# Performance work log

Measured on AMD Instinct MI355X. Metric: run time of the kernel, lower is better.

Reference implementation:

```python
import jax, jax.numpy as jnp
import numpy as np

N, L, C_IN, NOISE_C, COMP, NC = 64, 1024, 514, 64, 16, 3
MAIN_C = COMP + NOISE_C  # 80

def _conv1d(x, w, b):
    # x: [N, Cin, L], w: [Cout, Cin, K] -> 'same' padding conv, stride 1
    k = w.shape[-1]
    y = jax.lax.conv_general_dilated(x, w, (1,), [(k // 2, k // 2)],
                                     dimension_numbers=('NCH', 'OIH', 'NCH'))
    return y + b[None, :, None]

def _bn(x, gamma, beta, eps=1e-5):
    # training-mode BatchNorm1d: biased batch stats over (N, L)
    mu = jnp.mean(x, axis=(0, 2), keepdims=True)
    var = jnp.var(x, axis=(0, 2), keepdims=True)
    return (x - mu) * jax.lax.rsqrt(var + eps) * gamma[None, :, None] + beta[None, :, None]

def _lrelu(x):
    return jax.nn.leaky_relu(x, 0.2)

def _pos_encode(length, dim, dtype):
    d = jnp.arange(dim)
    div = 1.0 / jnp.power(10000.0, (2.0 * (d // 2).astype(dtype)) / dim)  # [dim]
    ang = div[:, None] * jnp.arange(length, dtype=dtype)[None, :]          # [dim, L]
    pe = jnp.where((d % 2 == 0)[:, None], jnp.sin(ang), jnp.cos(ang))
    return pe[None].astype(dtype)  # [1, dim, L]

def _label_revise(probs):
    # Vectorized equivalent of the per-sample Python revision loop
    # (circle_itv=2, slider_itv=4, stride=2). Output length == input length.
    # Row j semantics (m = 4*(j//4), chain(m) = pred[m]==2 and pred[m+4]==2 and m+4<L):
    #   j%4==0: always probs[j]
    #   chain(m) and j%4!=0: pad [0,0,1]
    #   j%4==1 (not chain): pred[m] in {1,2} -> [1,0,0] else probs[j]
    #   j%4==2 (not chain): probs[j]
    #   j%4==3 (not chain): pred[j-1]==1 -> [1,0,0] else probs[j]
    n, l, c = probs.shape
    pred = jnp.argmax(probs, axis=-1)                 # [N, L]
    pred_b = pred[:, ::4]                              # pred at multiples of 4
    nxt = jnp.concatenate([pred_b[:, 1:], jnp.full((n, 1), -1, pred_b.dtype)], axis=1)
    chain = jnp.repeat((pred_b == 2) & (nxt == 2), 4, axis=1)   # [N, L]
    predm = jnp.repeat(pred_b, 4, axis=1)                        # [N, L]
    phase = jnp.arange(l) % 4
    prev = jnp.concatenate([jnp.zeros((n, 1), pred.dtype), pred[:, :-1]], axis=1)
    pad100 = jnp.array([1.0, 0.0, 0.0], probs.dtype)
    pad001 = jnp.array([0.0, 0.0, 1.0], probs.dtype)
    c100 = (((phase == 1)[None] & ((predm == 1) | (predm == 2)))
            | ((phase == 3)[None] & (prev == 1))) & ~chain
    out = jnp.where(c100[..., None], pad100, probs)
    out = jnp.where((chain & (phase != 0)[None])[..., None], pad001, out)
    return out

def _forward(noise, cond_data, gumbel, ew1, eb1, ew2, eb2, eg, ebt,
             w3, b3, w4, b4, g4, bt4, lw1, lb1, lw2, lb2, lw3, lb3):
    # FeatureExtractor
    x = jnp.swapaxes(cond_data, 1, 2)                       # [N, 514, L]
    x = _lrelu(_conv1d(x, ew1, eb1))                        # [N, 32, L]
    cond = _bn(_conv1d(x, ew2, eb2), eg, ebt)               # [N, 16, L] (no act)
    # main generator
    gi = jnp.concatenate([cond, jnp.swapaxes(noise, 1, 2)], axis=1)  # [N, 80, L]
    gi = gi + _pos_encode(L, MAIN_C, gi.dtype)
    h = _lrelu(_conv1d(gi, w3, b3))                         # [N, 48, L]
    h = _lrelu(_bn(_conv1d(h, w4, b4), g4, bt4))            # [N, 12, L]
    h = h.reshape(h.shape[0], -1)                           # [N, 12*L]
    h = _lrelu(h @ lw1 + lb1)
    h = _lrelu(h @ lw2 + lb2)
    logits = (h @ lw3 + lb3).reshape(-1, L, NC)             # [N, L, 3]
    rev = _label_revise(logits)
    # hard gumbel-softmax (tau=1) with straight-through estimator
    y_soft = jax.nn.softmax(rev + gumbel, axis=-1)
    y_hard = jax.nn.one_hot(jnp.argmax(y_soft, axis=-1), NC, dtype=y_soft.dtype)
    gen = y_hard + y_soft - jax.lax.stop_gradient(y_soft)
    return gen, cond

def setup_inputs() -> dict:
    key = jax.random.key(0)
    ks = jax.random.split(key, 12)
    s = jnp.float32(0.02)
    return {
        'noise': jax.random.normal(ks[0], (N, L, NOISE_C), jnp.float32),
        'cond_data': jax.random.normal(ks[1], (N, L, C_IN), jnp.float32),
        'gumbel': jax.random.gumbel(ks[2], (N, L, NC), jnp.float32),
        'ew1': jax.random.normal(ks[3], (C_IN // 16, C_IN, 1), jnp.float32) * s,
        'eb1': jnp.zeros((C_IN // 16,), jnp.float32),
        'ew2': jax.random.normal(ks[4], (COMP, C_IN // 16, 3), jnp.float32) * s,
        'eb2': jnp.zeros((COMP,), jnp.float32),
        'eg': jnp.ones((COMP,), jnp.float32),
        'ebt': jnp.zeros((COMP,), jnp.float32),
        'w3': jax.random.normal(ks[5], (NC * 16, MAIN_C, 7), jnp.float32) * s,
        'b3': jnp.zeros((NC * 16,), jnp.float32),
        'w4': jax.random.normal(ks[6], (NC * 4, NC * 16, 3), jnp.float32) * s,
        'b4': jnp.zeros((NC * 4,), jnp.float32),
        'g4': jnp.ones((NC * 4,), jnp.float32),
        'bt4': jnp.zeros((NC * 4,), jnp.float32),
        'lw1': jax.random.normal(ks[7], (NC * 4 * L, NC * L), jnp.float32) * s,
        'lb1': jnp.zeros((NC * L,), jnp.float32),
        'lw2': jax.random.normal(ks[8], (NC * L, NC * L), jnp.float32) * s,
        'lb2': jnp.zeros((NC * L,), jnp.float32),
        'lw3': jax.random.normal(ks[9], (NC * L, NC * L), jnp.float32) * s,
        'lb3': jnp.zeros((NC * L,), jnp.float32),
    }

def reference(noise, cond_data, gumbel, ew1, eb1, ew2, eb2, eg, ebt,
              w3, b3, w4, b4, g4, bt4, lw1, lb1, lw2, lb2, lw3, lb3):
    return _forward(noise, cond_data, gumbel, ew1, eb1, ew2, eb2, eg, ebt,
                    w3, b3, w4, b4, g4, bt4, lw1, lb1, lw2, lb2, lw3, lb3)
```

## Files before the change

### kernel.cpp

```cpp
#include <hip/hip_runtime.h>
#include <hip/hip_bf16.h>
#include <math.h>


__device__ __forceinline__ float lrelu(float x){ return fmaxf(x, 0.2f*x); }

__global__ void k_init(const float* __restrict__ ew1, const float* __restrict__ ew2,
                       const float* __restrict__ w3,  const float* __restrict__ w4,
                       float* __restrict__ wT1, float* __restrict__ wT2,
                       float* __restrict__ wT3, float* __restrict__ wT4,
                       float* __restrict__ pe){
  int i = blockIdx.x*256 + threadIdx.x;
  if (i < 16448){
    int c = i>>5, oc = i&31;
    wT1[i] = ew1[oc*514 + c];
  } else if (i < 16448+1536){
    int j = i - 16448; int oc = j%16; int t = j/16; int dl = t%3; int ic = t/3;
    wT2[j] = ew2[(oc*32+ic)*3 + dl];
  } else if (i < 16448+1536+26880){
    int j = i - 17984; int oc = j%48; int t = j/48; int dl = t%7; int ic = t/7;
    wT3[j] = w3[(oc*80+ic)*7 + dl];
  } else if (i < 46592){
    int j = i - 44864; int oc = j%12; int t = j/12; int dl = t%3; int ic = t/3;
    wT4[j] = w4[(oc*48+ic)*3 + dl];
  } else if (i < 46592 + 80*1024){
    int j = i - 46592;
    int ch = j >> 10, l = j & 1023;
    double dv = 1.0 / pow(10000.0, (2.0*(double)(ch>>1)) / 80.0);
    double ang = dv * (double)l;
    pe[j] = (float)((ch & 1) ? cos(ang) : sin(ang));
  }
}

__global__ __launch_bounds__(256) void k_conv1(const float* __restrict__ A,
    const float* __restrict__ wT1, const float* __restrict__ eb1,
    float* __restrict__ x1){
  __shared__ float red[32][256];
  const int tid = threadIdx.x;
  const int pl  = tid & 63;
  const int s   = __builtin_amdgcn_readfirstlane(tid >> 6);
  const int p   = blockIdx.x*64 + pl;

  const int c0 = (s == 0) ? 0 : 130 + (s-1)*128;
  const int c1 = (s == 0) ? 130 : 130 + s*128;

  const float* row = A + (size_t)p*514;
  float acc[32];
  #pragma unroll
  for (int j=0;j<32;j++) acc[j]=0.f;

  #pragma unroll 8
  for (int c=c0;c<c1;c+=2){
    float2 v = *reinterpret_cast<const float2*>(row + c);
    const float* w = wT1 + (size_t)c*32;
    #pragma unroll
    for (int j=0;j<32;j++) acc[j] = fmaf(v.x, w[j],    acc[j]);
    #pragma unroll
    for (int j=0;j<32;j++) acc[j] = fmaf(v.y, w[32+j], acc[j]);
  }

  #pragma unroll
  for (int j=0;j<32;j++) red[j][s*64 + pl] = acc[j];
  __syncthreads();

  float out[8];
  #pragma unroll
  for (int j=0;j<8;j++){
    const int c = s*8 + j;
    float v = (red[c][pl] + red[c][64+pl]) + (red[c][128+pl] + red[c][192+pl]);
    out[j] = lrelu(v + eb1[c]);
  }
  float* dst = x1 + ((size_t)(blockIdx.x*64 + pl))*32 + s*8;
  *(float4*)(dst  ) = make_float4(out[0],out[1],out[2],out[3]);
  *(float4*)(dst+4) = make_float4(out[4],out[5],out[6],out[7]);
}

__global__ __launch_bounds__(256) void k_conv2(const float* __restrict__ x1,
    const float* __restrict__ wT2, const float* __restrict__ eb2,
    float* __restrict__ y2, float* __restrict__ part){
  __shared__ float xt[32][264];
  const int tid = threadIdx.x, lane = tid & 63;
  const int wv = __builtin_amdgcn_readfirstlane(tid >> 6);
  const int n = blockIdx.x >> 2, base = (blockIdx.x & 3)*256;

  for (int r = tid; r < 264; r += 256){
    int l = base - 4 + r;
    if (l >= 0 && l < 1024){
      const float* src = x1 + ((size_t)n*1024 + l)*32;
      #pragma unroll
      for (int c=0;c<32;c+=4){
        float4 v = *(const float4*)(src + c);
        xt[c][r]=v.x; xt[c+1][r]=v.y; xt[c+2][r]=v.z; xt[c+3][r]=v.w;
      }
    } else {
      #pragma unroll
      for (int c=0;c<32;c++) xt[c][r] = 0.f;
    }
  }
  __syncthreads();

  const int og = wv*4;
  const int j0 = 4*lane;
  float acc[4][4];
  #pragma unroll
  for (int j=0;j<4;j++){
    #pragma unroll
    for (int p=0;p<4;p++) acc[j][p]=0.f;
  }
  for (int ic=0; ic<32; ic++){
    float xr[12];
    #pragma unroll
    for (int u=0;u<12;u+=4){
      float4 v = *(const float4*)&xt[ic][j0+u];
      xr[u]=v.x; xr[u+1]=v.y; xr[u+2]=v.z; xr[u+3]=v.w;
    }
    const float* wrow = wT2 + ic*48 + og;
    #pragma unroll
    for (int dl=0;dl<3;dl++){
      #pragma unroll
      for (int j=0;j<4;j++){
        float w = wrow[dl*16 + j];
        #pragma unroll
        for (int p=0;p<4;p++)
          acc[j][p] = fmaf(xr[p+dl+3], w, acc[j][p]);
      }
    }
  }
  float s[4], q[4];
  #pragma unroll
  for (int j=0;j<4;j++){ s[j]=0.f; q[j]=0.f; }
  const int l0 = base + 4*lane;
  #pragma unroll
  for (int p=0;p<4;p++){
    float vv[4];
    #pragma unroll
    for (int j=0;j<4;j++){
      float val = acc[j][p] + eb2[og+j];
      vv[j]=val; s[j]+=val; q[j]+=val*val;
    }
    *(float4*)(y2 + ((size_t)n*1024 + l0 + p)*16 + og) = make_float4(vv[0],vv[1],vv[2],vv[3]);
  }
  #pragma unroll
  for (int off=32; off; off>>=1){
    #pragma unroll
    for (int j=0;j<4;j++){ s[j] += __shfl_xor(s[j], off); q[j] += __shfl_xor(q[j], off); }
  }
  if (lane == 0){
    #pragma unroll
    for (int j=0;j<4;j++){
      part[((size_t)blockIdx.x*16 + og + j)*2    ] = s[j];
      part[((size_t)blockIdx.x*16 + og + j)*2 + 1] = q[j];
    }
  }
}

__global__ __launch_bounds__(256) void k_gi(const float* __restrict__ y2,
    const float* __restrict__ noise, const float* __restrict__ pe,
    const float* __restrict__ bn2p, const float* __restrict__ eg,
    const float* __restrict__ ebt,
    float* __restrict__ gi, float* __restrict__ cond_out){
  __shared__ double pS[16][16], pQ[16][16];
  __shared__ float ssh[32];
  const int tid = threadIdx.x;
  {
    int c = tid & 15, chunk = tid >> 4;
    double S=0.0, Q=0.0;
    #pragma unroll 4
    for (int i=chunk*16; i<chunk*16+16; i++){
      S += (double)bn2p[((size_t)i*16 + c)*2];
      Q += (double)bn2p[((size_t)i*16 + c)*2 + 1];
    }
    pS[chunk][c] = S; pQ[chunk][c] = Q;
  }
  __syncthreads();
  if (tid < 16){
    double S=0.0, Q=0.0;
    #pragma unroll
    for (int k=0;k<16;k++){ S += pS[k][tid]; Q += pQ[k][tid]; }
    double mean = S / 65536.0;
    double var  = Q / 65536.0 - mean*mean;
    double sc   = (double)eg[tid] / sqrt(var + 1e-5);
    ssh[tid*2]   = (float)sc;
    ssh[tid*2+1] = (float)((double)ebt[tid] - mean*sc);
  }
  __syncthreads();

  int n = blockIdx.x >> 2;
  int l = (blockIdx.x & 3)*256 + tid;
  size_t p = (size_t)n*1024 + l;
  float* grow = gi + p*80;
  #pragma unroll
  for (int c=0;c<16;c++){
    float v  = y2[p*16 + c];
    float cv = fmaf(v, ssh[2*c], ssh[2*c+1]);
    cond_out[((size_t)n*16 + c)*1024 + l] = cv;
    grow[c] = cv + pe[c*1024 + l];
  }
  #pragma unroll
  for (int c=0;c<64;c++){
    grow[16+c] = noise[p*64 + c] + pe[(16+c)*1024 + l];
  }
}

__global__ __launch_bounds__(256) void k_conv3(const float* __restrict__ gi,
    const float* __restrict__ wT3, const float* __restrict__ b3,
    float* __restrict__ h3){
  __shared__ float xt[80][136];
  const int tid = threadIdx.x, lane = tid & 63;
  const int og = __builtin_amdgcn_readfirstlane(tid >> 6) * 12;
  const int n = blockIdx.x >> 3, base = (blockIdx.x & 7)*128;

  {
    const int half = tid & 1;
    for (int r = tid >> 1; r < 136; r += 128){
      int l = base - 4 + r;
      if (l >= 0 && l < 1024){
        const float* src = gi + ((size_t)n*1024 + l)*80 + half*40;
        #pragma unroll
        for (int c=0;c<40;c+=4){
          float4 v = *(const float4*)(src + c);
          xt[half*40+c][r]=v.x; xt[half*40+c+1][r]=v.y; xt[half*40+c+2][r]=v.z; xt[half*40+c+3][r]=v.w;
        }
      } else {
        #pragma unroll
        for (int c=0;c<40;c++) xt[half*40+c][r]=0.f;
      }
    }
  }
  __syncthreads();

  float acc[12][2];
  #pragma unroll
  for (int j=0;j<12;j++){ acc[j][0]=0.f; acc[j][1]=0.f; }
  const int j0 = 2*lane;
  for (int ic=0; ic<80; ic++){
    float xr[10];
    #pragma unroll
    for (int u=0;u<10;u+=2){
      float2 v = *(const float2*)&xt[ic][j0+u];
      xr[u]=v.x; xr[u+1]=v.y;
    }
    const float* wrow = wT3 + ic*336 + og;
    #pragma unroll
    for (int dl=0;dl<7;dl++){
      #pragma unroll
      for (int j=0;j<12;j++){
        float w = wrow[dl*48 + j];
        acc[j][0] = fmaf(xr[1+dl], w, acc[j][0]);
        acc[j][1] = fmaf(xr[2+dl], w, acc[j][1]);
      }
    }
  }
  const int l0 = base + 2*lane;
  #pragma unroll
  for (int p=0;p<2;p++){
    float v[12];
    #pragma unroll
    for (int j=0;j<12;j++) v[j] = lrelu(acc[j][p] + b3[og+j]);
    float* dst = h3 + ((size_t)n*1024 + l0 + p)*48 + og;
    *(float4*)(dst  ) = make_float4(v[0],v[1],v[2],v[3]);
    *(float4*)(dst+4) = make_float4(v[4],v[5],v[6],v[7]);
    *(float4*)(dst+8) = make_float4(v[8],v[9],v[10],v[11]);
  }
}

__global__ __launch_bounds__(256) void k_conv4(const float* __restrict__ h3,
    const float* __restrict__ wT4, const float* __restrict__ b4,
    float* __restrict__ y4, float* __restrict__ part){
  __shared__ float xt[48][258];
  __shared__ float red[4][24];
  const int tid = threadIdx.x, lane = tid & 63, wv = tid >> 6;
  const int n = blockIdx.x >> 2, base = (blockIdx.x & 3)*256;

  for (int r = tid; r < 258; r += 256){
    int l = base - 1 + r;
    if (l >= 0 && l < 1024){
      const float* src = h3 + ((size_t)n*1024 + l)*48;
      #pragma unroll
      for (int c=0;c<48;c+=4){
        float4 v = *(const float4*)(src + c);
        xt[c][r]=v.x; xt[c+1][r]=v.y; xt[c+2][r]=v.z; xt[c+3][r]=v.w;
      }
    } else {
      #pragma unroll
      for (int c=0;c<48;c++) xt[c][r]=0.f;
    }
  }
  __syncthreads();

  float acc[12];
  #pragma unroll
  for (int j=0;j<12;j++) acc[j]=0.f;
  for (int ic=0; ic<48; ic++){
    float x0 = xt[ic][tid], x1v = xt[ic][tid+1], x2 = xt[ic][tid+2];
    const float* wrow = wT4 + ic*36;
    #pragma unroll
    for (int j=0;j<12;j++){
      acc[j] = fmaf(x0,  wrow[j],      acc[j]);
      acc[j] = fmaf(x1v, wrow[12 + j], acc[j]);
      acc[j] = fmaf(x2,  wrow[24 + j], acc[j]);
    }
  }
  float s[12], q[12];
  #pragma unroll
  for (int j=0;j<12;j++){
    float v = acc[j] + b4[j];
    acc[j] = v; s[j] = v; q[j] = v*v;
  }
  {
    float* dst = y4 + ((size_t)n*1024 + base + tid)*12;
    *(float4*)(dst  ) = make_float4(acc[0],acc[1],acc[2],acc[3]);
    *(float4*)(dst+4) = make_float4(acc[4],acc[5],acc[6],acc[7]);
    *(float4*)(dst+8) = make_float4(acc[8],acc[9],acc[10],acc[11]);
  }
  #pragma unroll
  for (int off=32; off; off>>=1){
    #pragma unroll
    for (int j=0;j<12;j++){ s[j] += __shfl_xor(s[j], off); q[j] += __shfl_xor(q[j], off); }
  }
  if (lane == 0){
    #pragma unroll
    for (int j=0;j<12;j++){ red[wv][j] = s[j]; red[wv][12+j] = q[j]; }
  }
  __syncthreads();
  if (tid < 24){
    float v = red[0][tid] + red[1][tid] + red[2][tid] + red[3][tid];
    if (tid < 12) part[((size_t)blockIdx.x*12 + tid)*2] = v;
    else          part[((size_t)blockIdx.x*12 + (tid-12))*2 + 1] = v;
  }
}

__global__ __launch_bounds__(256) void k_hflat(const float* __restrict__ y4,
    const float* __restrict__ bn4p, const float* __restrict__ g4,
    const float* __restrict__ bt4, float* __restrict__ hT){
  __shared__ double pS[16][12], pQ[16][12];
  __shared__ float ssh[24];
  const int tid = threadIdx.x;
  if (tid < 192){
    int c = tid % 12, chunk = tid / 12;
    double S=0.0, Q=0.0;
    #pragma unroll 4
    for (int i=chunk*16; i<chunk*16+16; i++){
      S += (double)bn4p[((size_t)i*12 + c)*2];
      Q += (double)bn4p[((size_t)i*12 + c)*2 + 1];
    }
    pS[chunk][c] = S; pQ[chunk][c] = Q;
  }
  __syncthreads();
  if (tid < 12){
    double S=0.0, Q=0.0;
    #pragma unroll
    for (int k=0;k<16;k++){ S += pS[k][tid]; Q += pQ[k][tid]; }
    double mean = S / 65536.0;
    double var  = Q / 65536.0 - mean*mean;
    double sc   = (double)g4[tid] / sqrt(var + 1e-5);
    ssh[tid*2]   = (float)sc;
    ssh[tid*2+1] = (float)((double)bt4[tid] - mean*sc);
  }
  __syncthreads();

  int nn = tid & 63;
  int l  = blockIdx.x*4 + (tid >> 6);
  const float* src = y4 + ((size_t)nn*1024 + l)*12;
  #pragma unroll
  for (int c=0;c<12;c++){
    float v = lrelu(fmaf(src[c], ssh[2*c], ssh[2*c+1]));
    hT[((size_t)(c*1024 + l))*64 + nn] = v;
  }
}

__global__ __launch_bounds__(256) void k_fc2(const float* __restrict__ AT,
    const float* __restrict__ W, float* __restrict__ part,
    int nsplit, int kwave){
  __shared__ float red[64][64];
  const int lane = threadIdx.x & 63;
  const int w  = __builtin_amdgcn_readfirstlane(threadIdx.x >> 6);
  const int sk = w >> 1;
  const int mh = (w & 1) * 32;
  const int s  = blockIdx.x % nsplit;
  const int ot = blockIdx.x / nsplit;
  const int o  = ot*64 + lane;
  const int k0 = (s*2 + sk) * kwave;

  float acc[32];
  #pragma unroll
  for (int m=0;m<32;m++) acc[m]=0.f;

  const float* ap = AT + (size_t)k0*64 + mh;
  const float* wp = W  + (size_t)k0*3072 + o;

  float wb[8];
  #pragma unroll
  for (int u=0;u<8;u++) wb[u] = wp[(size_t)u*3072];

  for (int k=0; k<kwave-8; k+=8){
    float wn[8];
    const float* wpn = wp + (size_t)(k+8)*3072;
    #pragma unroll
    for (int u=0;u<8;u++) wn[u] = wpn[(size_t)u*3072];
    #pragma unroll
    for (int u=0;u<8;u++){
      const float* a = ap + (size_t)(k+u)*64;
      #pragma unroll
      for (int m=0;m<32;m++) acc[m] = fmaf(a[m], wb[u], acc[m]);
    }
    #pragma unroll
    for (int u=0;u<8;u++) wb[u] = wn[u];
  }
  #pragma unroll
  for (int u=0;u<8;u++){
    const float* a = ap + (size_t)(kwave-8+u)*64;
    #pragma unroll
    for (int m=0;m<32;m++) acc[m] = fmaf(a[m], wb[u], acc[m]);
  }

  if (sk == 1){
    #pragma unroll
    for (int m=0;m<32;m++) red[mh + m][lane] = acc[m];
  }
  __syncthreads();
  if (sk == 0){
    float* dst = part + (size_t)s*64*3072 + o;
    #pragma unroll
    for (int m=0;m<32;m++){
      acc[m] += red[mh + m][lane];
      dst[(size_t)(mh + m)*3072] = acc[m];
    }
  }
}

__global__ __launch_bounds__(256) void k_fcreduce(const float* __restrict__ part,
    const float* __restrict__ bias, float* __restrict__ out,
    int S, int act, int transposed){
  const int ot = blockIdx.x >> 4;
  const int mg = blockIdx.x & 15;
  const int lane = threadIdx.x & 63;
  const int o = ot*64 + lane;
  const int m = mg*4 + (threadIdx.x >> 6);
  float v = 0.f;
  for (int s=0;s<S;s++) v += part[((size_t)s*64 + m)*3072 + o];
  v += bias[o];
  if (act) v = fmaxf(v, 0.2f*v);
  if (transposed) out[(size_t)o*64 + m] = v;
  else            out[(size_t)m*3072 + o] = v;
}

__global__ __launch_bounds__(256) void k_label(const float* __restrict__ logits,
    const float* __restrict__ gumbel, float* __restrict__ out){
  __shared__ int pred[1024];
  const int n = blockIdx.x;
  const float* lg = logits + (size_t)n*3072;
  for (int l = threadIdx.x; l < 1024; l += 256){
    float a = lg[l*3], b = lg[l*3+1], c = lg[l*3+2];
    int pm = 0; float bv = a;
    if (b > bv){ pm = 1; bv = b; }
    if (c > bv){ pm = 2; }
    pred[l] = pm;
  }
  __syncthreads();
  const float* gm = gumbel + (size_t)n*3072;
  float* op = out + (size_t)n*3072;
  for (int l = threadIdx.x; l < 1024; l += 256){
    int phase = l & 3, lb = l >> 2;
    int pb  = pred[lb*4];
    int nxt = (lb < 255) ? pred[(lb+1)*4] : -1;
    bool chain = (pb == 2) && (nxt == 2);
    int prev = (l > 0) ? pred[l-1] : 0;
    bool c100 = (((phase == 1) && (pb == 1 || pb == 2)) ||
                 ((phase == 3) && (prev == 1))) && !chain;
    float r0, r1, r2;
    if (chain && phase != 0){ r0=0.f; r1=0.f; r2=1.f; }
    else if (c100)          { r0=1.f; r1=0.f; r2=0.f; }
    else { r0 = lg[l*3]; r1 = lg[l*3+1]; r2 = lg[l*3+2]; }
    float z0 = r0 + gm[l*3], z1 = r1 + gm[l*3+1], z2 = r2 + gm[l*3+2];
    int am = 0; float bv = z0;
    if (z1 > bv){ am = 1; bv = z1; }
    if (z2 > bv){ am = 2; }
    op[l*3+0] = (am == 0) ? 1.f : 0.f;
    op[l*3+1] = (am == 1) ? 1.f : 0.f;
    op[l*3+2] = (am == 2) ? 1.f : 0.f;
  }
}

extern "C" void kernel_launch(void* const* d_in, const int* in_sizes, int n_in,
                              void* d_out, int out_size, void* d_ws, size_t ws_size,
                              hipStream_t stream){
  (void)in_sizes; (void)n_in; (void)out_size;
  const float* noise     = (const float*)d_in[0];
  const float* cond_data = (const float*)d_in[1];
  const float* gumbel    = (const float*)d_in[2];
  const float* ew1 = (const float*)d_in[3];
  const float* eb1 = (const float*)d_in[4];
  const float* ew2 = (const float*)d_in[5];
  const float* eb2 = (const float*)d_in[6];
  const float* eg  = (const float*)d_in[7];
  const float* ebt = (const float*)d_in[8];
  const float* w3  = (const float*)d_in[9];
  const float* b3  = (const float*)d_in[10];
  const float* w4  = (const float*)d_in[11];
  const float* b4  = (const float*)d_in[12];
  const float* g4  = (const float*)d_in[13];
  const float* bt4 = (const float*)d_in[14];
  const float* lw1 = (const float*)d_in[15];
  const float* lb1 = (const float*)d_in[16];
  const float* lw2 = (const float*)d_in[17];
  const float* lb2 = (const float*)d_in[18];
  const float* lw3 = (const float*)d_in[19];
  const float* lb3 = (const float*)d_in[20];

  float* ws = (float*)d_ws;
  float* wT1   = ws + 0;
  float* wT2   = ws + 16448;
  float* wT3   = ws + 17984;
  float* wT4   = ws + 44864;
  float* pe    = ws + 46592;
  float* bn2p  = ws + 128512;
  float* bn4p  = ws + 136736;
  float* x1    = ws + 143360;
  float* y2    = ws + 2240512;
  float* h3    = ws + 143360;
  float* gi    = ws + 3289088;
  float* y4    = ws + 3289088;
  float* hT    = ws + 4075520;
  float* fcp   = ws + 4861952;

  int S1 = 32;
  if (ws_size < (size_t)(4861952 + 32*196608 + 3*196608) * 4) S1 = 16;
  const int S23 = 16;
  float* fc1T  = fcp + (size_t)S1*196608;
  float* fc2T  = fc1T + 196608;
  float* logi  = fc2T + 196608;
  const int kw1  = 12288 / (S1*2);
  const int kw23 = 3072 / (S23*2);

  float* out_gen  = (float*)d_out;
  float* out_cond = (float*)d_out + 196608;

  k_init <<<502, 256, 0, stream>>>(ew1, ew2, w3, w4, wT1, wT2, wT3, wT4, pe);
  k_conv1<<<1024, 256, 0, stream>>>(cond_data, wT1, eb1, x1);
  k_conv2<<<256, 256, 0, stream>>>(x1, wT2, eb2, y2, bn2p);
  k_gi   <<<256, 256, 0, stream>>>(y2, noise, pe, bn2p, eg, ebt, gi, out_cond);
  k_conv3<<<512, 256, 0, stream>>>(gi, wT3, b3, h3);
  k_conv4<<<256, 256, 0, stream>>>(h3, wT4, b4, y4, bn4p);
  k_hflat<<<256, 256, 0, stream>>>(y4, bn4p, g4, bt4, hT);
  k_fc2  <<<48*S1, 256, 0, stream>>>(hT,   lw1, fcp, S1, kw1);
  k_fcreduce<<<768, 256, 0, stream>>>(fcp, lb1, fc1T, S1, 1, 1);
  k_fc2  <<<48*S23, 256, 0, stream>>>(fc1T, lw2, fcp, S23, kw23);
  k_fcreduce<<<768, 256, 0, stream>>>(fcp, lb2, fc2T, S23, 1, 1);
  k_fc2  <<<48*S23, 256, 0, stream>>>(fc2T, lw3, fcp, S23, kw23);
  k_fcreduce<<<768, 256, 0, stream>>>(fcp, lb3, logi, S23, 0, 0);
  k_label<<<64, 256, 0, stream>>>(logi, gumbel, out_gen);
}
```

Baseline: 344.3 us.

## Fuse BN-apply/positional-encoding into conv3 and deepen FC weight prefetch

Merges the k_gi kernel (BN2 normalisation, positional encoding add, noise concat) into the conv3 kernel's shared-memory tile load, which removes the intermediate gi buffer write and read. Conv3 now uses 64-position tiles with one output per lane over 1024 blocks, and each block recomputes the BN statistics reduction. The FC GEMM kernel prefetches 16 weight rows per step instead of 8. The workspace layout is reshuffled so h3 no longer aliases x1. Costs are redundant BN stat work in every block, more halo overhead, and higher register pressure in the FC kernel.

```diff
diff --git a/kernel.cpp b/kernel.cpp
--- a/kernel.cpp
+++ b/kernel.cpp
@@ -154,14 +154,19 @@
   }
 }
 
-__global__ __launch_bounds__(256) void k_gi(const float* __restrict__ y2,
+__global__ __launch_bounds__(256) void k_conv3(const float* __restrict__ y2,
     const float* __restrict__ noise, const float* __restrict__ pe,
     const float* __restrict__ bn2p, const float* __restrict__ eg,
     const float* __restrict__ ebt,
-    float* __restrict__ gi, float* __restrict__ cond_out){
+    const float* __restrict__ wT3, const float* __restrict__ b3,
+    float* __restrict__ h3, float* __restrict__ cond_out){
+  __shared__ float xt[80][72];
   __shared__ double pS[16][16], pQ[16][16];
   __shared__ float ssh[32];
-  const int tid = threadIdx.x;
+  const int tid = threadIdx.x, lane = tid & 63;
+  const int og = __builtin_amdgcn_readfirstlane(tid >> 6) * 12;
+  const int n = blockIdx.x >> 4, base = (blockIdx.x & 15)*64;
+
   {
     int c = tid & 15, chunk = tid >> 4;
     double S=0.0, Q=0.0;
@@ -185,79 +190,66 @@
   }
   __syncthreads();
 
-  int n = blockIdx.x >> 2;
-  int l = (blockIdx.x & 3)*256 + tid;
-  size_t p = (size_t)n*1024 + l;
-  float* grow = gi + p*80;
-  #pragma unroll
-  for (int c=0;c<16;c++){
-    float v  = y2[p*16 + c];
-    float cv = fmaf(v, ssh[2*c], ssh[2*c+1]);
-    cond_out[((size_t)n*16 + c)*1024 + l] = cv;
-    grow[c] = cv + pe[c*1024 + l];
-  }
-  #pragma unroll
-  for (int c=0;c<64;c++){
-    grow[16+c] = noise[p*64 + c] + pe[(16+c)*1024 + l];
-  }
-}
-
-__global__ __launch_bounds__(256) void k_conv3(const float* __restrict__ gi,
-    const float* __restrict__ wT3, const float* __restrict__ b3,
-    float* __restrict__ h3){
-  __shared__ float xt[80][136];
-  const int tid = threadIdx.x, lane = tid & 63;
-  const int og = __builtin_amdgcn_readfirstlane(tid >> 6) * 12;
-  const int n = blockIdx.x >> 3, base = (blockIdx.x & 7)*128;
-
   {
-    const int half = tid & 1;
-    for (int r = tid >> 1; r < 136; r += 128){
+    const int q = tid & 3;
+    for (int r = tid >> 2; r < 72; r += 64){
       int l = base - 4 + r;
-      if (l >= 0 && l < 1024){
-        const float* src = gi + ((size_t)n*1024 + l)*80 + half*40;
-        #pragma unroll
-        for (int c=0;c<40;c+=4){
-          float4 v = *(const float4*)(src + c);
-          xt[half*40+c][r]=v.x; xt[half*40+c+1][r]=v.y; xt[half*40+c+2][r]=v.z; xt[half*40+c+3][r]=v.w;
+      bool valid = (l >= 0 && l < 1024);
+      if (q == 0){
+        if (valid){
+          size_t p = (size_t)n*1024 + l;
+          const float* ys = y2 + p*16;
+          bool interior = (r >= 4 && r < 68);
+          #pragma unroll
+          for (int c=0;c<16;c++){
+            float cv = fmaf(ys[c], ssh[2*c], ssh[2*c+1]);
+            if (interior) cond_out[((size_t)n*16 + c)*1024 + l] = cv;
+            xt[c][r] = cv + pe[c*1024 + l];
+          }
+          const float* ns = noise + p*64;
+          #pragma unroll
+          for (int c=0;c<4;c++)
+            xt[16+c][r] = ns[c] + pe[(16+c)*1024 + l];
+        } else {
+          #pragma unroll
+          for (int c=0;c<20;c++) xt[c][r] = 0.f;
         }
       } else {
-        #pragma unroll
-        for (int c=0;c<40;c++) xt[half*40+c][r]=0.f;
+        if (valid){
+          size_t p = (size_t)n*1024 + l;
+          const float* ns = noise + p*64 + (q*20 - 16);
+          #pragma unroll
+          for (int c=0;c<20;c++)
+            xt[q*20 + c][r] = ns[c] + pe[(q*20 + c)*1024 + l];
+        } else {
+          #pragma unroll
+          for (int c=0;c<20;c++) xt[q*20 + c][r] = 0.f;
+        }
       }
     }
   }
   __syncthreads();
 
-  float acc[12][2];
-  #pragma unroll
-  for (int j=0;j<12;j++){ acc[j][0]=0.f; acc[j][1]=0.f; }
-  const int j0 = 2*lane;
+  float acc[12];
+  #pragma unroll
+  for (int j=0;j<12;j++) acc[j]=0.f;
   for (int ic=0; ic<80; ic++){
-    float xr[10];
-    #pragma unroll
-    for (int u=0;u<10;u+=2){
-      float2 v = *(const float2*)&xt[ic][j0+u];
-      xr[u]=v.x; xr[u+1]=v.y;
-    }
+    float xr[7];
+    #pragma unroll
+    for (int u=0;u<7;u++) xr[u] = xt[ic][lane+1+u];
     const float* wrow = wT3 + ic*336 + og;
     #pragma unroll
     for (int dl=0;dl<7;dl++){
       #pragma unroll
-      for (int j=0;j<12;j++){
-        float w = wrow[dl*48 + j];
-        acc[j][0] = fmaf(xr[1+dl], w, acc[j][0]);
-        acc[j][1] = fmaf(xr[2+dl], w, acc[j][1]);
-      }
-    }
-  }
-  const int l0 = base + 2*lane;
-  #pragma unroll
-  for (int p=0;p<2;p++){
+      for (int j=0;j<12;j++)
+        acc[j] = fmaf(xr[dl], wrow[dl*48 + j], acc[j]);
+    }
+  }
+  {
     float v[12];
     #pragma unroll
-    for (int j=0;j<12;j++) v[j] = lrelu(acc[j][p] + b3[og+j]);
-    float* dst = h3 + ((size_t)n*1024 + l0 + p)*48 + og;
+    for (int j=0;j<12;j++) v[j] = lrelu(acc[j] + b3[og+j]);
+    float* dst = h3 + ((size_t)n*1024 + base + lane)*48 + og;
     *(float4*)(dst  ) = make_float4(v[0],v[1],v[2],v[3]);
     *(float4*)(dst+4) = make_float4(v[4],v[5],v[6],v[7]);
     *(float4*)(dst+8) = make_float4(v[8],v[9],v[10],v[11]);
@@ -389,27 +381,27 @@
   const float* ap = AT + (size_t)k0*64 + mh;
   const float* wp = W  + (size_t)k0*3072 + o;
 
-  float wb[8];
-  #pragma unroll
-  for (int u=0;u<8;u++) wb[u] = wp[(size_t)u*3072];
-
-  for (int k=0; k<kwave-8; k+=8){
-    float wn[8];
-    const float* wpn = wp + (size_t)(k+8)*3072;
-    #pragma unroll
-    for (int u=0;u<8;u++) wn[u] = wpn[(size_t)u*3072];
-    #pragma unroll
-    for (int u=0;u<8;u++){
+  float wb[16];
+  #pragma unroll
+  for (int u=0;u<16;u++) wb[u] = wp[(size_t)u*3072];
+
+  for (int k=0; k<kwave-16; k+=16){
+    float wn[16];
+    const float* wpn = wp + (size_t)(k+16)*3072;
+    #pragma unroll
+    for (int u=0;u<16;u++) wn[u] = wpn[(size_t)u*3072];
+    #pragma unroll
+    for (int u=0;u<16;u++){
       const float* a = ap + (size_t)(k+u)*64;
       #pragma unroll
       for (int m=0;m<32;m++) acc[m] = fmaf(a[m], wb[u], acc[m]);
     }
     #pragma unroll
-    for (int u=0;u<8;u++) wb[u] = wn[u];
-  }
-  #pragma unroll
-  for (int u=0;u<8;u++){
-    const float* a = ap + (size_t)(kwave-8+u)*64;
+    for (int u=0;u<16;u++) wb[u] = wn[u];
+  }
+  #pragma unroll
+  for (int u=0;u<16;u++){
+    const float* a = ap + (size_t)(kwave-16+u)*64;
     #pragma unroll
     for (int m=0;m<32;m++) acc[m] = fmaf(a[m], wb[u], acc[m]);
   }
@@ -518,14 +510,13 @@
   float* bn4p  = ws + 136736;
   float* x1    = ws + 143360;
   float* y2    = ws + 2240512;
-  float* h3    = ws + 143360;
-  float* gi    = ws + 3289088;
-  float* y4    = ws + 3289088;
-  float* hT    = ws + 4075520;
-  float* fcp   = ws + 4861952;
+  float* h3    = ws + 3289088;
+  float* y4    = ws + 6434816;
+  float* hT    = ws + 7221248;
+  float* fcp   = ws + 8007680;
 
   int S1 = 32;
-  if (ws_size < (size_t)(4861952 + 32*196608 + 3*196608) * 4) S1 = 16;
+  if (ws_size < (size_t)(8007680 + 32*196608 + 3*196608) * 4) S1 = 16;
   const int S23 = 16;
   float* fc1T  = fcp + (size_t)S1*196608;
   float* fc2T  = fc1T + 196608;
@@ -539,8 +530,7 @@
   k_init <<<502, 256, 0, stream>>>(ew1, ew2, w3, w4, wT1, wT2, wT3, wT4, pe);
   k_conv1<<<1024, 256, 0, stream>>>(cond_data, wT1, eb1, x1);
   k_conv2<<<256, 256, 0, stream>>>(x1, wT2, eb2, y2, bn2p);
-  k_gi   <<<256, 256, 0, stream>>>(y2, noise, pe, bn2p, eg, ebt, gi, out_cond);
-  k_conv3<<<512, 256, 0, stream>>>(gi, wT3, b3, h3);
+  k_conv3<<<1024, 256, 0, stream>>>(y2, noise, pe, bn2p, eg, ebt, wT3, b3, h3, out_cond);
   k_conv4<<<256, 256, 0, stream>>>(h3, wT4, b4, y4, bn4p);
   k_hflat<<<256, 256, 0, stream>>>(y4, bn4p, g4, bt4, hT);
   k_fc2  <<<48*S1, 256, 0, stream>>>(hT,   lw1, fcp, S1, kw1);
```

After: 360.1 us. 4.6% more time.
